# Performance work log

Measured on AMD Instinct MI355X. Metric: run time of the kernel, lower is better.

## Reference

```python
import jax, jax.numpy as jnp
import numpy as np

LOG_2PI = float(np.log(2.0 * np.pi))


def setup_inputs() -> dict:
    key = jax.random.key(0)
    k1, k2, k3 = jax.random.split(key, 3)
    B, C, D = 256, 1000, 256
    return {
        "x": jax.random.normal(k1, (B, D), dtype=jnp.float32),
        "metric_tensor": jax.random.normal(k2, (B, D, D), dtype=jnp.float32),
        "log_priors": jnp.zeros((C,), dtype=jnp.float32),
        "class_means": jax.random.normal(k3, (C, D), dtype=jnp.float32),
        "class_log_vars": jnp.zeros((C, D), dtype=jnp.float32),
    }


def reference(x, metric_tensor, log_priors, class_means, class_log_vars):
    D = x.shape[-1]
    # diff: [B, C, D]
    diff = x[:, None, :] - class_means[None, :, :]
    # Mahalanobis quadratic form per (batch, class): diff^T G diff
    maha = jnp.einsum("bcd,bde,bce->bc", diff, metric_tensor, diff)
    log_likelihood = -0.5 * (maha + jnp.sum(class_log_vars, axis=-1)[None, :] + D * LOG_2PI)
    log_posteriors = log_likelihood + log_priors[None, :]
    return jax.nn.log_softmax(log_posteriors, axis=-1)
```

## Files before the change

### kernel.cpp

```cpp
#include <hip/hip_runtime.h>

#define LOG2PI 1.83787706640934548356f

typedef __attribute__((ext_vector_type(4))) float f32x4;
typedef __attribute__((ext_vector_type(2))) float f32x2;
typedef __attribute__((ext_vector_type(8))) short bf16x8;

__device__ __forceinline__ unsigned short f2bf(float f) {
    union { float f; unsigned u; } v; v.f = f;
    unsigned r = v.u + 0x7fffu + ((v.u >> 16) & 1u);
    return (unsigned short)(r >> 16);
}
__device__ __forceinline__ float bf2f(unsigned short h) {
    union { unsigned u; float f; } v; v.u = ((unsigned)h) << 16; return v.f;
}
__device__ __forceinline__ bf16x8 pack8(f32x4 a, f32x4 b) {
    bf16x8 h;
    h[0]=(short)f2bf(a[0]); h[1]=(short)f2bf(a[1]); h[2]=(short)f2bf(a[2]); h[3]=(short)f2bf(a[3]);
    h[4]=(short)f2bf(b[0]); h[5]=(short)f2bf(b[1]); h[6]=(short)f2bf(b[2]); h[7]=(short)f2bf(b[3]);
    return h;
}
__device__ __forceinline__ float rowsum16(float v) {
    v += __int_as_float(__builtin_amdgcn_update_dpp(0, __float_as_int(v), 0x111, 0xf, 0xf, true));
    v += __int_as_float(__builtin_amdgcn_update_dpp(0, __float_as_int(v), 0x112, 0xf, 0xf, true));
    v += __int_as_float(__builtin_amdgcn_update_dpp(0, __float_as_int(v), 0x114, 0xf, 0xf, true));
    v += __int_as_float(__builtin_amdgcn_update_dpp(0, __float_as_int(v), 0x118, 0xf, 0xf, true));
    return v;
}

__global__ __launch_bounds__(256)
void k_prep(const float* __restrict__ clv, const float* __restrict__ lp,
            float* __restrict__ bias)
{
    const int w = threadIdx.x >> 6, lane = threadIdx.x & 63;
    const int c = blockIdx.x * 4 + w;
    if (c >= 1000) return;
    f32x4 v = *reinterpret_cast<const f32x4*>(clv + c * 256 + lane * 4);
    float s = v[0] + v[1] + v[2] + v[3];
    #pragma unroll
    for (int m = 1; m < 64; m <<= 1) s += __shfl_xor(s, m);
    if (lane == 0) bias[c] = lp[c] - 0.5f * (s + 256.0f * LOG2PI);
}

__global__ __launch_bounds__(512, 4)
void k_main(const float* __restrict__ x, const float* __restrict__ G,
            const float* __restrict__ means, float* __restrict__ maha_ws)
{
    __shared__ char dbuf[2][16384];
    __shared__ float maha[1024];

    const int b    = blockIdx.x >> 1;
    const int q    = blockIdx.x & 1;
    const int tid  = threadIdx.x;
    const int lane = tid & 63;
    const int wave = tid >> 6;
    const int wm   = wave >> 2;
    const int wn   = wave & 3;
    const int lrow = lane & 15;
    const int g    = lane >> 4;
    const int d0   = q * 128;

    const float* Gb = G + (size_t)b * 65536;
    const float* xb = x + b * 256;

    maha[tid] = 0.f; maha[tid + 512] = 0.f;

    bf16x8 greg[2][8];
    #pragma unroll
    for (int n = 0; n < 2; ++n) {
        const float* rowp = Gb + (size_t)(d0 + wn * 32 + n * 16 + lrow) * 256 + g * 8;
        #pragma unroll
        for (int ks = 0; ks < 8; ++ks) {
            f32x4 v0 = *reinterpret_cast<const f32x4*>(rowp + ks * 32);
            f32x4 v1 = *reinterpret_cast<const f32x4*>(rowp + ks * 32 + 4);
            greg[n][ks] = pack8(v0, v1);
        }
    }

    const int sr = tid & 31;
    const int ss = tid >> 5;
    const f32x4 x0a = *reinterpret_cast<const f32x4*>(xb + ss * 8);
    const f32x4 x0b = *reinterpret_cast<const f32x4*>(xb + ss * 8 + 4);
    const f32x4 x1a = *reinterpret_cast<const f32x4*>(xb + (ss + 16) * 8);
    const f32x4 x1b = *reinterpret_cast<const f32x4*>(xb + (ss + 16) * 8 + 4);

    f32x4 r0a, r0b, r1a, r1b;
    auto load_chunk = [&](int c0) {
        int cc = c0 + sr; if (cc > 999) cc = 999;
        const float* mp = means + (size_t)cc * 256;
        r0a = *reinterpret_cast<const f32x4*>(mp + ss * 8);
        r0b = *reinterpret_cast<const f32x4*>(mp + ss * 8 + 4);
        r1a = *reinterpret_cast<const f32x4*>(mp + (ss + 16) * 8);
        r1b = *reinterpret_cast<const f32x4*>(mp + (ss + 16) * 8 + 4);
    };
    auto write_chunk = [&](int bufi) {
        *reinterpret_cast<bf16x8*>(dbuf[bufi] + (ss * 32 + sr) * 16)        = pack8(x0a - r0a, x0b - r0b);
        *reinterpret_cast<bf16x8*>(dbuf[bufi] + ((ss + 16) * 32 + sr) * 16) = pack8(x1a - r1a, x1b - r1b);
    };

    load_chunk(0);

    for (int t = 0; t < 32; ++t) {
        write_chunk(t & 1);
        __syncthreads();
        if (t < 31) load_chunk((t + 1) * 32);

        const char* buf = dbuf[t & 1];
        f32x4 acc[2];
        acc[0] = f32x4{0.f, 0.f, 0.f, 0.f};
        acc[1] = f32x4{0.f, 0.f, 0.f, 0.f};

        #pragma unroll
        for (int ks = 0; ks < 8; ++ks) {
            bf16x8 afr = *reinterpret_cast<const bf16x8*>(
                buf + ((ks * 4 + g) * 32 + wm * 16 + lrow) * 16);
            acc[0] = __builtin_amdgcn_mfma_f32_16x16x32_bf16(afr, greg[0][ks], acc[0], 0, 0, 0);
            acc[1] = __builtin_amdgcn_mfma_f32_16x16x32_bf16(afr, greg[1][ks], acc[1], 0, 0, 0);
        }

        float p[4] = {0.f, 0.f, 0.f, 0.f};
        #pragma unroll
        for (int n = 0; n < 2; ++n) {
            const int col = d0 + wn * 32 + n * 16 + lrow;
            const char* dp = buf + ((col >> 3) * 32) * 16 + (col & 7) * 2;
            #pragma unroll
            for (int i = 0; i < 4; ++i) {
                const int row = wm * 16 + g * 4 + i;
                p[i] += acc[n][i] * bf2f(*reinterpret_cast<const unsigned short*>(dp + row * 16));
            }
        }
        #pragma unroll
        for (int i = 0; i < 4; ++i) p[i] = rowsum16(p[i]);
        if (lrow == 15) {
            const int c = t * 32 + wm * 16 + g * 4;
            #pragma unroll
            for (int i = 0; i < 4; ++i)
                if (c + i < 1000) atomicAdd(&maha[c + i], p[i]);
        }
    }

    __syncthreads();
    for (int i = tid; i < 1000; i += 512)
        atomicAdd(&maha_ws[(size_t)b * 1000 + i], maha[i]);
}

__global__ __launch_bounds__(256)
void k_soft(const float* __restrict__ maha_ws, const float* __restrict__ bias,
            float* __restrict__ out)
{
    __shared__ float red[4];
    const int b = blockIdx.x, tid = threadIdx.x;
    const int lane = tid & 63, w = tid >> 6;
    float s[4];
    float mx = -3.4e38f;
    #pragma unroll
    for (int i = 0; i < 4; ++i) {
        const int c = tid + i * 256;
        if (c < 1000) {
            float v = -0.5f * maha_ws[(size_t)b * 1000 + c] + bias[c];
            s[i] = v; mx = fmaxf(mx, v);
        } else s[i] = -3.4e38f;
    }
    #pragma unroll
    for (int m = 1; m < 64; m <<= 1) mx = fmaxf(mx, __shfl_xor(mx, m));
    if (lane == 0) red[w] = mx;
    __syncthreads();
    const float bm = fmaxf(fmaxf(red[0], red[1]), fmaxf(red[2], red[3]));
    __syncthreads();
    float se = 0.f;
    #pragma unroll
    for (int i = 0; i < 4; ++i) {
        const int c = tid + i * 256;
        if (c < 1000) se += expf(s[i] - bm);
    }
    #pragma unroll
    for (int m = 1; m < 64; m <<= 1) se += __shfl_xor(se, m);
    if (lane == 0) red[w] = se;
    __syncthreads();
    const float lse = bm + logf(red[0] + red[1] + red[2] + red[3]);
    #pragma unroll
    for (int i = 0; i < 4; ++i) {
        const int c = tid + i * 256;
        if (c < 1000) out[(size_t)b * 1000 + c] = s[i] - lse;
    }
}

extern "C" void kernel_launch(void* const* d_in, const int* in_sizes, int n_in,
                              void* d_out, int out_size, void* d_ws, size_t ws_size,
                              hipStream_t stream)
{
    const float* x     = (const float*)d_in[0];
    const float* G     = (const float*)d_in[1];
    const float* lp    = (const float*)d_in[2];
    const float* means = (const float*)d_in[3];
    const float* clv   = (const float*)d_in[4];
    float* out     = (float*)d_out;
    float* maha_ws = (float*)d_ws;
    float* bias    = (float*)d_ws + 256 * 1000;

    hipMemsetAsync(maha_ws, 0, (size_t)256 * 1000 * sizeof(float), stream);
    k_prep<<<250, 256, 0, stream>>>(clv, lp, bias);
    k_main<<<512, 512, 0, stream>>>(x, G, means, maha_ws);
    k_soft<<<256, 256, 0, stream>>>(maha_ws, bias, out);
}
```

Before: 188.7 us.

## Split work by class groups with full-D G per block and swizzled LDS

Each block now covers one batch row and a 256-class slice and holds the full 256x256 G in registers across four waves, instead of one half of D for all classes. Because each block owns its classes outright, the global atomics, the memset and the workspace buffer are gone, and partial Mahalanobis sums go straight into the output buffer for the softmax kernel to read. It also swaps the MFMA operand roles so the reduction runs across lanes with two shuffles instead of DPP row sums, and XOR-swizzles the LDS layout to avoid bank conflicts. G is now read from memory four times per batch instead of twice, and the heavier per-thread register footprint limits occupancy to about two blocks.

```diff
diff --git a/kernel.cpp b/kernel.cpp
--- a/kernel.cpp
+++ b/kernel.cpp
@@ -3,29 +3,19 @@
 #define LOG2PI 1.83787706640934548356f
 
 typedef __attribute__((ext_vector_type(4))) float f32x4;
-typedef __attribute__((ext_vector_type(2))) float f32x2;
 typedef __attribute__((ext_vector_type(8))) short bf16x8;
+typedef __attribute__((ext_vector_type(2))) unsigned int u32x2;
 
 __device__ __forceinline__ unsigned short f2bf(float f) {
     union { float f; unsigned u; } v; v.f = f;
     unsigned r = v.u + 0x7fffu + ((v.u >> 16) & 1u);
     return (unsigned short)(r >> 16);
 }
-__device__ __forceinline__ float bf2f(unsigned short h) {
-    union { unsigned u; float f; } v; v.u = ((unsigned)h) << 16; return v.f;
-}
 __device__ __forceinline__ bf16x8 pack8(f32x4 a, f32x4 b) {
     bf16x8 h;
     h[0]=(short)f2bf(a[0]); h[1]=(short)f2bf(a[1]); h[2]=(short)f2bf(a[2]); h[3]=(short)f2bf(a[3]);
     h[4]=(short)f2bf(b[0]); h[5]=(short)f2bf(b[1]); h[6]=(short)f2bf(b[2]); h[7]=(short)f2bf(b[3]);
     return h;
-}
-__device__ __forceinline__ float rowsum16(float v) {
-    v += __int_as_float(__builtin_amdgcn_update_dpp(0, __float_as_int(v), 0x111, 0xf, 0xf, true));
-    v += __int_as_float(__builtin_amdgcn_update_dpp(0, __float_as_int(v), 0x112, 0xf, 0xf, true));
-    v += __int_as_float(__builtin_amdgcn_update_dpp(0, __float_as_int(v), 0x114, 0xf, 0xf, true));
-    v += __int_as_float(__builtin_amdgcn_update_dpp(0, __float_as_int(v), 0x118, 0xf, 0xf, true));
-    return v;
 }
 
 __global__ __launch_bounds__(256)
@@ -42,33 +32,31 @@
     if (lane == 0) bias[c] = lp[c] - 0.5f * (s + 256.0f * LOG2PI);
 }
 
-__global__ __launch_bounds__(512, 4)
+__global__ __launch_bounds__(256, 2)
 void k_main(const float* __restrict__ x, const float* __restrict__ G,
-            const float* __restrict__ means, float* __restrict__ maha_ws)
+            const float* __restrict__ means, float* __restrict__ out)
 {
-    __shared__ char dbuf[2][16384];
-    __shared__ float maha[1024];
+    __shared__ char dbuf[2][8192];
+    __shared__ float maha[256];
 
-    const int b    = blockIdx.x >> 1;
-    const int q    = blockIdx.x & 1;
-    const int tid  = threadIdx.x;
-    const int lane = tid & 63;
-    const int wave = tid >> 6;
-    const int wm   = wave >> 2;
-    const int wn   = wave & 3;
-    const int lrow = lane & 15;
-    const int g    = lane >> 4;
-    const int d0   = q * 128;
+    const int b     = blockIdx.x >> 2;
+    const int cg    = blockIdx.x & 3;
+    const int cbase = cg * 256;
+    const int tid   = threadIdx.x;
+    const int lane  = tid & 63;
+    const int wn    = tid >> 6;
+    const int lrow  = lane & 15;
+    const int g     = lane >> 4;
 
     const float* Gb = G + (size_t)b * 65536;
     const float* xb = x + b * 256;
 
-    maha[tid] = 0.f; maha[tid + 512] = 0.f;
+    maha[tid] = 0.f;
 
-    bf16x8 greg[2][8];
+    bf16x8 greg[4][8];
     #pragma unroll
-    for (int n = 0; n < 2; ++n) {
-        const float* rowp = Gb + (size_t)(d0 + wn * 32 + n * 16 + lrow) * 256 + g * 8;
+    for (int n = 0; n < 4; ++n) {
+        const float* rowp = Gb + (size_t)(wn * 64 + n * 16 + lrow) * 256 + g * 8;
         #pragma unroll
         for (int ks = 0; ks < 8; ++ks) {
             f32x4 v0 = *reinterpret_cast<const f32x4*>(rowp + ks * 32);
@@ -77,76 +65,76 @@
         }
     }
 
-    const int sr = tid & 31;
-    const int ss = tid >> 5;
-    const f32x4 x0a = *reinterpret_cast<const f32x4*>(xb + ss * 8);
-    const f32x4 x0b = *reinterpret_cast<const f32x4*>(xb + ss * 8 + 4);
-    const f32x4 x1a = *reinterpret_cast<const f32x4*>(xb + (ss + 16) * 8);
-    const f32x4 x1b = *reinterpret_cast<const f32x4*>(xb + (ss + 16) * 8 + 4);
+    const int sr = tid & 15;
+    const int s0 = tid >> 4;
+    const int e0 = s0 * 8, e1 = e0 + 128;
+    const f32x4 xa0 = *reinterpret_cast<const f32x4*>(xb + e0);
+    const f32x4 xa1 = *reinterpret_cast<const f32x4*>(xb + e0 + 4);
+    const f32x4 xb0 = *reinterpret_cast<const f32x4*>(xb + e1);
+    const f32x4 xb1 = *reinterpret_cast<const f32x4*>(xb + e1 + 4);
+    const int wbyte0 = (s0 * 16 + (sr ^ ((s0 & 3) << 1))) * 16;
+    const int wbyte1 = wbyte0 + 4096;
 
     f32x4 r0a, r0b, r1a, r1b;
     auto load_chunk = [&](int c0) {
-        int cc = c0 + sr; if (cc > 999) cc = 999;
+        int cc = cbase + c0 + sr; if (cc > 999) cc = 999;
         const float* mp = means + (size_t)cc * 256;
-        r0a = *reinterpret_cast<const f32x4*>(mp + ss * 8);
-        r0b = *reinterpret_cast<const f32x4*>(mp + ss * 8 + 4);
-        r1a = *reinterpret_cast<const f32x4*>(mp + (ss + 16) * 8);
-        r1b = *reinterpret_cast<const f32x4*>(mp + (ss + 16) * 8 + 4);
+        r0a = *reinterpret_cast<const f32x4*>(mp + e0);
+        r0b = *reinterpret_cast<const f32x4*>(mp + e0 + 4);
+        r1a = *reinterpret_cast<const f32x4*>(mp + e1);
+        r1b = *reinterpret_cast<const f32x4*>(mp + e1 + 4);
     };
     auto write_chunk = [&](int bufi) {
-        *reinterpret_cast<bf16x8*>(dbuf[bufi] + (ss * 32 + sr) * 16)        = pack8(x0a - r0a, x0b - r0b);
-        *reinterpret_cast<bf16x8*>(dbuf[bufi] + ((ss + 16) * 32 + sr) * 16) = pack8(x1a - r1a, x1b - r1b);
+        *reinterpret_cast<bf16x8*>(dbuf[bufi] + wbyte0) = pack8(xa0 - r0a, xa1 - r0b);
+        *reinterpret_cast<bf16x8*>(dbuf[bufi] + wbyte1) = pack8(xb0 - r1a, xb1 - r1b);
     };
 
     load_chunk(0);
 
-    for (int t = 0; t < 32; ++t) {
+    for (int t = 0; t < 16; ++t) {
         write_chunk(t & 1);
         __syncthreads();
-        if (t < 31) load_chunk((t + 1) * 32);
+        if (t < 15) load_chunk((t + 1) * 16);
 
         const char* buf = dbuf[t & 1];
-        f32x4 acc[2];
-        acc[0] = f32x4{0.f, 0.f, 0.f, 0.f};
-        acc[1] = f32x4{0.f, 0.f, 0.f, 0.f};
+        f32x4 acc[4];
+        #pragma unroll
+        for (int n = 0; n < 4; ++n) acc[n] = f32x4{0.f, 0.f, 0.f, 0.f};
 
         #pragma unroll
         for (int ks = 0; ks < 8; ++ks) {
-            bf16x8 afr = *reinterpret_cast<const bf16x8*>(
-                buf + ((ks * 4 + g) * 32 + wm * 16 + lrow) * 16);
-            acc[0] = __builtin_amdgcn_mfma_f32_16x16x32_bf16(afr, greg[0][ks], acc[0], 0, 0, 0);
-            acc[1] = __builtin_amdgcn_mfma_f32_16x16x32_bf16(afr, greg[1][ks], acc[1], 0, 0, 0);
+            bf16x8 bfr = *reinterpret_cast<const bf16x8*>(
+                buf + ((4 * ks + g) * 16 + (lrow ^ (g << 1))) * 16);
+            #pragma unroll
+            for (int n = 0; n < 4; ++n)
+                acc[n] = __builtin_amdgcn_mfma_f32_16x16x32_bf16(greg[n][ks], bfr, acc[n], 0, 0, 0);
         }
 
-        float p[4] = {0.f, 0.f, 0.f, 0.f};
+        float p = 0.f;
         #pragma unroll
-        for (int n = 0; n < 2; ++n) {
-            const int col = d0 + wn * 32 + n * 16 + lrow;
-            const char* dp = buf + ((col >> 3) * 32) * 16 + (col & 7) * 2;
-            #pragma unroll
-            for (int i = 0; i < 4; ++i) {
-                const int row = wm * 16 + g * 4 + i;
-                p[i] += acc[n][i] * bf2f(*reinterpret_cast<const unsigned short*>(dp + row * 16));
-            }
+        for (int n = 0; n < 4; ++n) {
+            const int d  = wn * 64 + n * 16 + g * 4;
+            const int se = d >> 3;
+            const int byte = (se * 16 + (lrow ^ ((se & 3) << 1))) * 16 + (d & 7) * 2;
+            u32x2 dv = *reinterpret_cast<const u32x2*>(buf + byte);
+            const float f0 = __uint_as_float(dv[0] << 16);
+            const float f1 = __uint_as_float(dv[0] & 0xffff0000u);
+            const float f2 = __uint_as_float(dv[1] << 16);
+            const float f3 = __uint_as_float(dv[1] & 0xffff0000u);
+            p += acc[n][0] * f0 + acc[n][1] * f1 + acc[n][2] * f2 + acc[n][3] * f3;
         }
-        #pragma unroll
-        for (int i = 0; i < 4; ++i) p[i] = rowsum16(p[i]);
-        if (lrow == 15) {
-            const int c = t * 32 + wm * 16 + g * 4;
-            #pragma unroll
-            for (int i = 0; i < 4; ++i)
-                if (c + i < 1000) atomicAdd(&maha[c + i], p[i]);
-        }
+        p += __shfl_xor(p, 16);
+        p += __shfl_xor(p, 32);
+        if (lane < 16) atomicAdd(&maha[t * 16 + lrow], p);
     }
 
     __syncthreads();
-    for (int i = tid; i < 1000; i += 512)
-        atomicAdd(&maha_ws[(size_t)b * 1000 + i], maha[i]);
+    const int c = cbase + tid;
+    if (c < 1000) out[(size_t)b * 1000 + c] = maha[tid];
 }
 
 __global__ __launch_bounds__(256)
-void k_soft(const float* __restrict__ maha_ws, const float* __restrict__ bias,
-            float* __restrict__ out)
+void k_soft(const float* __restrict__ bias, float* __restrict__ out)
 {
     __shared__ float red[4];
     const int b = blockIdx.x, tid = threadIdx.x;
@@ -157,7 +145,7 @@
     for (int i = 0; i < 4; ++i) {
         const int c = tid + i * 256;
         if (c < 1000) {
-            float v = -0.5f * maha_ws[(size_t)b * 1000 + c] + bias[c];
+            float v = -0.5f * out[(size_t)b * 1000 + c] + bias[c];
             s[i] = v; mx = fmaxf(mx, v);
         } else s[i] = -3.4e38f;
     }
@@ -194,12 +182,10 @@
     const float* lp    = (const float*)d_in[2];
     const float* means = (const float*)d_in[3];
     const float* clv   = (const float*)d_in[4];
-    float* out     = (float*)d_out;
-    float* maha_ws = (float*)d_ws;
-    float* bias    = (float*)d_ws + 256 * 1000;
+    float* out  = (float*)d_out;
+    float* bias = (float*)d_ws;
 
-    hipMemsetAsync(maha_ws, 0, (size_t)256 * 1000 * sizeof(float), stream);
     k_prep<<<250, 256, 0, stream>>>(clv, lp, bias);
-    k_main<<<512, 512, 0, stream>>>(x, G, means, maha_ws);
-    k_soft<<<256, 256, 0, stream>>>(maha_ws, bias, out);
+    k_main<<<1024, 256, 0, stream>>>(x, G, means, out);
+    k_soft<<<256, 256, 0, stream>>>(bias, out);
 }
```

New measurement: 182.7 us. 3.2% less time.
